# Kernel tuning notes

Hardware: AMD Instinct MI355X
Metric: run time of the kernel (lower is better)

Reference implementation:

```python
import jax, jax.numpy as jnp
import numpy as np
import math

SCORE_THRESH = 0.05
NMS_THRESH = 0.5
DETS_PER_IMG = 100
IMG_W = 512.0
IMG_H = 512.0
BBOX_XFORM_CLIP = math.log(1000.0 / 16.0)
WEIGHTS = (10.0, 10.0, 5.0, 5.0)
NEG_INF = jnp.float32(-1e30)


def decode(rel, boxes):
    TO_REMOVE = 1.0
    w = boxes[:, 2] - boxes[:, 0] + TO_REMOVE
    h = boxes[:, 3] - boxes[:, 1] + TO_REMOVE
    cx = boxes[:, 0] + 0.5 * w
    cy = boxes[:, 1] + 0.5 * h
    wx, wy, ww, wh = WEIGHTS
    dx = rel[:, 0::4] / wx
    dy = rel[:, 1::4] / wy
    dw = jnp.minimum(rel[:, 2::4] / ww, BBOX_XFORM_CLIP)
    dh = jnp.minimum(rel[:, 3::4] / wh, BBOX_XFORM_CLIP)
    pcx = dx * w[:, None] + cx[:, None]
    pcy = dy * h[:, None] + cy[:, None]
    pw = jnp.exp(dw) * w[:, None]
    ph = jnp.exp(dh) * h[:, None]
    x1 = pcx - 0.5 * pw
    y1 = pcy - 0.5 * ph
    x2 = pcx + 0.5 * pw - 1.0
    y2 = pcy + 0.5 * ph - 1.0
    return jnp.stack([x1, y1, x2, y2], axis=-1)


def pairwise_iou(b):
    # b: [N,4] xyxy -> [N,N] IoU (with +1 box-size convention, matching _box_nms)
    area = (b[:, 2] - b[:, 0] + 1.0) * (b[:, 3] - b[:, 1] + 1.0)
    xx1 = jnp.maximum(b[:, None, 0], b[None, :, 0])
    yy1 = jnp.maximum(b[:, None, 1], b[None, :, 1])
    xx2 = jnp.minimum(b[:, None, 2], b[None, :, 2])
    yy2 = jnp.minimum(b[:, None, 3], b[None, :, 3])
    inter = jnp.maximum(xx2 - xx1 + 1.0, 0.0) * jnp.maximum(yy2 - yy1 + 1.0, 0.0)
    return inter / (area[:, None] + area[None, :] - inter)


def _process_image(logits, regr, props):
    # logits: [N,2], regr: [N,8], props: [N,4]
    N = logits.shape[0]
    probs = jax.nn.softmax(logits, axis=-1)
    dec = decode(regr, props)            # [N, 2, 4]
    boxes = dec[:, 1, :]                  # fg (lesion) class boxes
    scores = probs[:, 1]                  # fg scores
    # clip_to_image(remove_empty=False)
    boxes = jnp.stack([
        jnp.clip(boxes[:, 0], 0.0, IMG_W - 1.0),
        jnp.clip(boxes[:, 1], 0.0, IMG_H - 1.0),
        jnp.clip(boxes[:, 2], 0.0, IMG_W - 1.0),
        jnp.clip(boxes[:, 3], 0.0, IMG_H - 1.0)], axis=-1)
    valid = scores > SCORE_THRESH
    # sort by score descending, invalid (below-threshold) boxes last
    order = jnp.argsort(-jnp.where(valid, scores, NEG_INF))
    boxes_s = boxes[order]
    scores_s = scores[order]
    valid_s = valid[order]
    iou = pairwise_iou(boxes_s)           # [N,N]
    idxs = jnp.arange(N)
    def body(i, keep):
        # box i (if still kept) suppresses all later overlapping boxes
        sup = keep[i] & (iou[i] > NMS_THRESH) & (idxs > i)
        return keep & ~sup
    keep = jax.lax.fori_loop(0, N, body, valid_s)
    # keep top detections_per_img by score among surviving boxes
    final = jnp.where(keep, scores_s, NEG_INF)
    top_scores, top_idx = jax.lax.top_k(final, DETS_PER_IMG)
    top_valid = keep[top_idx]
    top_boxes = jnp.where(top_valid[:, None], boxes_s[top_idx], 0.0)
    top_scores = jnp.where(top_valid, top_scores, 0.0)
    out = jnp.concatenate([top_boxes, top_scores[:, None]], axis=-1)  # [D, 5]
    labels = jnp.where(top_valid, 1, 0).astype(jnp.int32)
    return out, labels, top_valid


def setup_inputs() -> dict:
    key = jax.random.key(0)
    kl, kr, kp = jax.random.split(key, 3)
    B, N = 16, 4096
    class_logits = jax.random.normal(kl, (B, N, 2), dtype=jnp.float32)
    box_regression = jax.random.normal(kr, (B, N, 8), dtype=jnp.float32)
    raw = jax.random.uniform(kp, (B, N, 4), dtype=jnp.float32)
    x1 = raw[..., 0] * (IMG_W - 72.0)
    y1 = raw[..., 1] * (IMG_H - 72.0)
    bw = raw[..., 2] * 56.0 + 8.0
    bh = raw[..., 3] * 56.0 + 8.0
    proposals = jnp.stack([x1, y1, x1 + bw, y1 + bh], axis=-1)
    return {"class_logits": class_logits, "box_regression": box_regression, "proposals": proposals}


def reference(class_logits, box_regression, proposals):
    # returns (detections [B, D, 5] = xyxy+score, labels [B, D], valid [B, D])
    return jax.vmap(_process_image)(class_logits, box_regression, proposals)
```

## Files before the change

### kernel.cpp

```cpp
#include <hip/hip_runtime.h>
#include <math.h>

#define NTHREADS 512
#define MAXN 4096
#define PER 8
#define DETS 100
#define CHUNK 256
#define CAP 512
#define NWAVES (NTHREADS / 64)

static __device__ __forceinline__ unsigned long long shfl_bc64(unsigned long long x, int src) {
    int lo = __shfl((int)(unsigned)x, src, 64);
    int hi = __shfl((int)(unsigned)(x >> 32), src, 64);
    return ((unsigned long long)(unsigned)hi << 32) | (unsigned)lo;
}

static __device__ __forceinline__ float iou_f(float ax1, float ay1, float ax2, float ay2, float aar,
                                              float bx1, float by1, float bx2, float by2, float bar) {
#pragma clang fp contract(off)
    float xx1 = fmaxf(ax1, bx1), yy1 = fmaxf(ay1, by1);
    float xx2 = fminf(ax2, bx2), yy2 = fminf(ay2, by2);
    float iw = fmaxf((xx2 - xx1) + 1.0f, 0.0f);
    float ih = fmaxf((yy2 - yy1) + 1.0f, 0.0f);
    float inter = iw * ih;
    return inter / ((aar + bar) - inter);
}

__global__ __launch_bounds__(NTHREADS) void postproc_kernel(
    const float* __restrict__ logits,
    const float* __restrict__ regr,
    const float* __restrict__ props,
    float* __restrict__ out,
    int B, int N)
{
#pragma clang fp contract(off)
    const int b    = blockIdx.x;
    const int tid  = threadIdx.x;
    const int lane = tid & 63;
    const int wid  = tid >> 6;

    __shared__ __align__(16) unsigned long long keysel[CAP];
    __shared__ unsigned hist4k[4096];
    __shared__ unsigned s_super[64];
    __shared__ float bx1s[CAP], by1s[CAP], bx2s[CAP], by2s[CAP], bars[CAP], bscs[CAP];
    __shared__ float kb[5][DETS + 64];
    __shared__ unsigned tmask[64][2];
    __shared__ unsigned supk[64];
    __shared__ int s_kept, s_cnt, s_C;
    __shared__ unsigned long long s_prefix, s_T;
    __shared__ int s_target, s_done, s_findkey;

    const float* lg = logits + (size_t)b * N * 2;
    const float* rg = regr   + (size_t)b * N * 8;
    const float* pp = props  + (size_t)b * N * 4;

    unsigned long long v[PER];
#pragma unroll
    for (int s = 0; s < PER; ++s) {
        int a = s * NTHREADS + tid;
        unsigned long long key;
        if (a < N) {
            float2 l = ((const float2*)lg)[a];
            float zmax = fmaxf(l.x, l.y), zmin = fminf(l.x, l.y);
            float e   = (float)exp((double)(zmin - zmax));
            float den = e + 1.0f;
            float sscore = (l.y >= l.x) ? (1.0f / den) : (e / den);
            float f = (sscore > 0.05f) ? sscore : -1e30f;
            unsigned u = __float_as_uint(f);
            u = (u & 0x80000000u) ? ~u : (u | 0x80000000u);
            key = ((unsigned long long)(~u) << 32) | (unsigned)a;
        } else key = ~0ull;
        v[s] = key;
    }
    if (tid == 0) s_kept = 0;

    float* obox = out + (size_t)b * DETS * 5;
    float* olab = out + (size_t)B * DETS * 5 + (size_t)b * DETS;
    float* oval = out + (size_t)B * DETS * 5 + (size_t)B * DETS + (size_t)b * DETS;
    const float CLIPV = (float)4.135166556742356;

    int kept = 0;

    while (kept < DETS) {
        for (int i = tid; i < 4096; i += NTHREADS) hist4k[i] = 0u;
        if (tid == 0) { s_cnt = 0; s_C = 0; }
        __syncthreads();

#pragma unroll
        for (int s = 0; s < PER; ++s) {
            unsigned hb = (unsigned)(v[s] >> 50) - 0x1000u;
            if (hb > 4094u) hb = 4095u;
            atomicAdd(&hist4k[hb], 1u);
        }
        __syncthreads();

        {
            unsigned p = 0;
            int base8 = tid * 8;
#pragma unroll
            for (int u = 0; u < 8; ++u) p += hist4k[base8 + u];
#pragma unroll
            for (int off = 4; off; off >>= 1) p += __shfl_down(p, off, 8);
            if ((tid & 7) == 0) s_super[tid >> 3] = p;
        }
        __syncthreads();

        if (tid < 64) {
            int l = tid;
            int sp = (int)s_super[l];
            int incl = sp;
#pragma unroll
            for (int off = 1; off < 64; off <<= 1) {
                int y = __shfl_up(incl, off, 64);
                if (l >= off) incl += y;
            }
            int total = __shfl(incl, 63, 64);
            int inv   = (int)hist4k[4095];
            int W     = total - inv;
            if (W > 0) {
                int tgt2 = W < CHUNK ? W : CHUNK;
                int excl = incl - sp;
                bool hit = (excl < tgt2) && (tgt2 <= incl);
                unsigned long long bm = __ballot(hit);
                int E = __ffsll(bm) - 1;
                int prevCum = __shfl(excl, E, 64);
                int c2 = (int)hist4k[E * 64 + l];
                int incl2 = c2;
#pragma unroll
                for (int off = 1; off < 64; off <<= 1) {
                    int y = __shfl_up(incl2, off, 64);
                    if (l >= off) incl2 += y;
                }
                int cum2 = prevCum + incl2;
                int excl2 = cum2 - c2;
                bool hit2 = (excl2 < tgt2) && (tgt2 <= cum2);
                if (hit2) {
                    int bin = E * 64 + l;
                    unsigned k32end = ((0x1000u + (unsigned)bin + 1u) << 18) - 1u;
                    s_T = ((unsigned long long)k32end << 32) | 0xFFFFFFFFull;
                    s_C = cum2;
                    s_target = tgt2;
                }
            }
        }
        __syncthreads();
        int C = s_C;
        if (C == 0) break;

        if (C > CAP) {
            unsigned (*histw)[256] = (unsigned(*)[256])hist4k;
            if (tid == 0) { s_prefix = 0ull; s_done = 0; s_findkey = 0; }
            for (int round = 0; round < 10; ++round) {
                __syncthreads();
                if (s_done) break;
                int sh = 56 - 8 * round;
                if (s_findkey) {
                    unsigned long long want = s_prefix; int shh = sh + 8;
#pragma unroll
                    for (int s = 0; s < PER; ++s)
                        if ((v[s] >> shh) == want) { s_T = v[s]; s_done = 1; }
                    continue;
                }
                for (int i = tid; i < NWAVES * 256; i += NTHREADS) ((unsigned*)histw)[i] = 0u;
                __syncthreads();
                unsigned long long pfx = s_prefix;
#pragma unroll
                for (int s = 0; s < PER; ++s) {
                    unsigned long long k = v[s];
                    bool match = (round == 0) || ((k >> (sh + 8)) == pfx);
                    if (match) atomicAdd(&histw[wid][(unsigned)((k >> sh) & 0xFFull)], 1u);
                }
                __syncthreads();
                if (tid < 64) {
                    int l = tid;
                    unsigned c0 = 0, c1 = 0, c2 = 0, c3 = 0;
#pragma unroll
                    for (int w2 = 0; w2 < NWAVES; ++w2) {
                        c0 += histw[w2][4*l+0]; c1 += histw[w2][4*l+1];
                        c2 += histw[w2][4*l+2]; c3 += histw[w2][4*l+3];
                    }
                    unsigned q0 = c0, q1 = q0 + c1, q2 = q1 + c2, q3 = q2 + c3;
                    int lanesum = (int)q3, incl = lanesum;
#pragma unroll
                    for (int off = 1; off < 64; off <<= 1) {
                        int y = __shfl_up(incl, off, 64);
                        if (l >= off) incl += y;
                    }
                    unsigned excl = (unsigned)(incl - lanesum);
                    unsigned tg = (unsigned)s_target;
                    if ((excl < tg) && (tg <= (unsigned)incl)) {
                        unsigned within = tg - excl;
                        int u_; unsigned below, bc;
                        if      (within <= q0) { u_ = 0; below = excl;      bc = c0; }
                        else if (within <= q1) { u_ = 1; below = excl + q0; bc = c1; }
                        else if (within <= q2) { u_ = 2; below = excl + q1; bc = c2; }
                        else                   { u_ = 3; below = excl + q2; bc = c3; }
                        unsigned long long npfx = (pfx << 8) | (unsigned)(4*l + u_);
                        s_target = (int)(tg - below);
                        if (sh == 0) { s_T = npfx; s_done = 1; }
                        else { s_prefix = npfx; if (bc == 1u) s_findkey = 1; }
                    }
                }
            }
            __syncthreads();
        }
        unsigned long long T = s_T;

#pragma unroll
        for (int s = 0; s < PER; ++s) {
            unsigned long long k = v[s];
            bool m = (k <= T);
            unsigned long long mask = __ballot(m);
            int basep = 0;
            if (lane == 0 && mask) basep = atomicAdd(&s_cnt, (int)__popcll(mask));
            basep = __shfl(basep, 0, 64);
            if (m) {
                int off = (int)__popcll(mask & ((1ull << lane) - 1ull));
                keysel[basep + off] = k;
                v[s] = ~0ull;
            }
        }
        __syncthreads();
        int cnt = s_cnt;

        if (tid < cnt) {
            unsigned long long myk = keysel[tid];
            unsigned idx = (unsigned)(myk & 0xFFFFFFFFull);
            float2 l  = ((const float2*)lg)[idx];
            float4 p  = ((const float4*)pp)[idx];
            float4 rr = *(const float4*)(rg + (size_t)idx * 8 + 4);
            int r = 0;
            const ulonglong2* kp2 = (const ulonglong2*)keysel;
            int half = cnt >> 1;
            for (int j = 0; j < half; ++j) {
                ulonglong2 two = kp2[j];
                r += (two.x < myk) ? 1 : 0;
                r += (two.y < myk) ? 1 : 0;
            }
            if (cnt & 1) r += (keysel[cnt - 1] < myk) ? 1 : 0;
            float zmax = fmaxf(l.x, l.y), zmin = fminf(l.x, l.y);
            float e = (float)exp((double)(zmin - zmax));
            float den = e + 1.0f;
            float sv = (l.y >= l.x) ? (1.0f / den) : (e / den);
            float w  = (p.z - p.x) + 1.0f;
            float h  = (p.w - p.y) + 1.0f;
            float cx = p.x + 0.5f * w;
            float cy = p.y + 0.5f * h;
            float dx = rr.x / 10.0f;
            float dy = rr.y / 10.0f;
            float dw = fminf(rr.z / 5.0f, CLIPV);
            float dh = fminf(rr.w / 5.0f, CLIPV);
            float pcx = dx * w + cx;
            float pcy = dy * h + cy;
            float ew = (float)exp((double)dw);
            float eh = (float)exp((double)dh);
            float pw = ew * w;
            float ph = eh * h;
            float x1 = pcx - 0.5f * pw;
            float y1 = pcy - 0.5f * ph;
            float x2 = (pcx + 0.5f * pw) - 1.0f;
            float y2 = (pcy + 0.5f * ph) - 1.0f;
            x1 = fminf(fmaxf(x1, 0.0f), 511.0f);
            y1 = fminf(fmaxf(y1, 0.0f), 511.0f);
            x2 = fminf(fmaxf(x2, 0.0f), 511.0f);
            y2 = fminf(fmaxf(y2, 0.0f), 511.0f);
            bx1s[r] = x1; by1s[r] = y1; bx2s[r] = x2; by2s[r] = y2;
            bars[r] = ((x2 - x1) + 1.0f) * ((y2 - y1) + 1.0f);
            bscs[r] = sv;
        }
        __syncthreads();

        for (int i0 = 0; i0 < cnt && kept < DETS; i0 += 64) {
            if (tid < 64) supk[tid] = (i0 + tid < cnt) ? 0u : 1u;
            else if (tid < 192) { int q = tid - 64; tmask[q >> 1][q & 1] = 0u; }
            __syncthreads();

            {
                int cc = tid & 63, sl = tid >> 6;
                if (supk[cc] == 0u) {
                    int gi = i0 + cc;
                    float x1 = bx1s[gi], y1 = by1s[gi], x2 = bx2s[gi], y2 = by2s[gi], ar = bars[gi];
                    for (int s2 = sl; s2 < kept; s2 += 8) {
                        float iou = iou_f(kb[0][s2], kb[1][s2], kb[2][s2], kb[3][s2], kb[4][s2],
                                          x1, y1, x2, y2, ar);
                        if (iou > 0.5f) { supk[cc] = 1u; break; }
                    }
                }
            }
            {
                int i = tid >> 3, jb = (tid & 7) << 3;
                int gi = i0 + i;
                float x1 = bx1s[gi], y1 = by1s[gi], x2 = bx2s[gi], y2 = by2s[gi], ar = bars[gi];
                unsigned byte = 0;
#pragma unroll
                for (int u = 0; u < 8; ++u) {
                    int j = jb + u;
                    if (j > i) {
                        int gj = i0 + j;
                        float iou = iou_f(x1, y1, x2, y2, ar,
                                          bx1s[gj], by1s[gj], bx2s[gj], by2s[gj], bars[gj]);
                        if (iou > 0.5f) byte |= (1u << u);
                    }
                }
                if (byte) atomicOr(&tmask[i][jb >> 5], byte << (jb & 31));
            }
            __syncthreads();

            if (tid < 64) {
                int l = tid;
                unsigned long long row = ((unsigned long long)tmask[l][1] << 32) | tmask[l][0];
                int alive0 = supk[l] ? 0 : 1;
                unsigned long long aliveMask = __ballot(alive0);
                unsigned long long pend = __ballot(alive0 && row != 0ull);
                while (pend) {
                    int c = __ffsll(pend) - 1;
                    unsigned long long rc = shfl_bc64(row, c);
                    aliveMask &= ~rc;
                    pend &= ~(1ull << c);
                    pend &= aliveMask;
                }
                int alive = (int)((aliveMask >> l) & 1ull);
                int rank = kept + (int)__popcll(aliveMask & ((1ull << l) - 1ull));
                int gi = i0 + l;
                if (alive) {
                    if (rank < DETS) {
                        float* o = obox + rank * 5;
                        o[0] = bx1s[gi]; o[1] = by1s[gi]; o[2] = bx2s[gi]; o[3] = by2s[gi];
                        o[4] = bscs[gi];
                        olab[rank] = 1.0f;
                        oval[rank] = 1.0f;
                    }
                    kb[0][rank] = bx1s[gi]; kb[1][rank] = by1s[gi];
                    kb[2][rank] = bx2s[gi]; kb[3][rank] = by2s[gi];
                    kb[4][rank] = bars[gi];
                }
                if (l == 0) s_kept = kept + (int)__popcll(aliveMask);
            }
            __syncthreads();
            kept = s_kept;
        }
    }

    int start = kept < DETS ? kept : DETS;
    for (int c2 = start + tid; c2 < DETS; c2 += NTHREADS) {
        float* o = obox + c2 * 5;
        o[0] = 0.0f; o[1] = 0.0f; o[2] = 0.0f; o[3] = 0.0f; o[4] = 0.0f;
        olab[c2] = 0.0f;
        oval[c2] = 0.0f;
    }
}

extern "C" void kernel_launch(void* const* d_in, const int* in_sizes, int n_in,
                              void* d_out, int out_size, void* d_ws, size_t ws_size,
                              hipStream_t stream) {
    (void)d_ws; (void)ws_size; (void)n_in;
    const float* logits = (const float*)d_in[0];
    const float* regr   = (const float*)d_in[1];
    const float* props  = (const float*)d_in[2];
    float* out = (float*)d_out;

    int B = out_size / 700;
    if (B < 1) B = 1;
    int N = in_sizes[0] / (2 * B);

    postproc_kernel<<<B, NTHREADS, 0, stream>>>(logits, regr, props, out, B, N);
}
```

Before: 21.26 us.

## Process whole 256-candidate chunk with single IoU matrix and bitmask NMS pass

Replaces the per-64-candidate NMS sub-loop with one pass over the entire candidate chunk (up to 256). All threads build a 256x256 upper-triangular suppression bitmask and check against already-kept boxes in the same barrier phase, and a single wave then resolves survivors with early exit once 100 detections are reached. The threshold selection now picks the largest bin prefix that fits within the chunk, falling back to the radix refine only when the first bin alone overflows. This cuts barrier rounds and serial chunk iterations, at the cost of more IoU work per chunk and 64-bit shared atomics.

```diff
diff --git a/kernel.cpp b/kernel.cpp
--- a/kernel.cpp
+++ b/kernel.cpp
@@ -5,15 +5,8 @@
 #define MAXN 4096
 #define PER 8
 #define DETS 100
-#define CHUNK 256
-#define CAP 512
+#define CMAX 256
 #define NWAVES (NTHREADS / 64)
-
-static __device__ __forceinline__ unsigned long long shfl_bc64(unsigned long long x, int src) {
-    int lo = __shfl((int)(unsigned)x, src, 64);
-    int hi = __shfl((int)(unsigned)(x >> 32), src, 64);
-    return ((unsigned long long)(unsigned)hi << 32) | (unsigned)lo;
-}
 
 static __device__ __forceinline__ float iou_f(float ax1, float ay1, float ax2, float ay2, float aar,
                                               float bx1, float by1, float bx2, float by2, float bar) {
@@ -39,14 +32,15 @@
     const int lane = tid & 63;
     const int wid  = tid >> 6;
 
-    __shared__ __align__(16) unsigned long long keysel[CAP];
+    __shared__ __align__(16) unsigned long long keysel[CMAX];
     __shared__ unsigned hist4k[4096];
     __shared__ unsigned s_super[64];
-    __shared__ float bx1s[CAP], by1s[CAP], bx2s[CAP], by2s[CAP], bars[CAP], bscs[CAP];
-    __shared__ float kb[5][DETS + 64];
-    __shared__ unsigned tmask[64][2];
-    __shared__ unsigned supk[64];
-    __shared__ int s_kept, s_cnt, s_C;
+    __shared__ unsigned long long rowmask[CMAX][4];
+    __shared__ unsigned rowNZ[CMAX];
+    __shared__ unsigned supk[CMAX];
+    __shared__ float bx1s[CMAX], by1s[CMAX], bx2s[CMAX], by2s[CMAX], bars[CMAX], bscs[CMAX];
+    __shared__ float kb[5][DETS + 4];
+    __shared__ int s_kept, s_cnt, s_C, s_fb;
     __shared__ unsigned long long s_prefix, s_T;
     __shared__ int s_target, s_done, s_findkey;
 
@@ -83,7 +77,7 @@
 
     while (kept < DETS) {
         for (int i = tid; i < 4096; i += NTHREADS) hist4k[i] = 0u;
-        if (tid == 0) { s_cnt = 0; s_C = 0; }
+        if (tid == 0) { s_cnt = 0; s_C = 0; s_fb = 0; }
         __syncthreads();
 
 #pragma unroll
@@ -107,47 +101,55 @@
 
         if (tid < 64) {
             int l = tid;
-            int sp = (int)s_super[l];
+            int inv = (int)hist4k[4095];
+            int sp = (int)s_super[l] - ((l == 63) ? inv : 0);
             int incl = sp;
 #pragma unroll
             for (int off = 1; off < 64; off <<= 1) {
                 int y = __shfl_up(incl, off, 64);
                 if (l >= off) incl += y;
             }
-            int total = __shfl(incl, 63, 64);
-            int inv   = (int)hist4k[4095];
-            int W     = total - inv;
+            int W = __shfl(incl, 63, 64);
             if (W > 0) {
-                int tgt2 = W < CHUNK ? W : CHUNK;
+                int tgt2 = W < CMAX ? W : CMAX;
                 int excl = incl - sp;
-                bool hit = (excl < tgt2) && (tgt2 <= incl);
+                bool hit = (excl <= tgt2) && (incl > tgt2);
                 unsigned long long bm = __ballot(hit);
-                int E = __ffsll(bm) - 1;
-                int prevCum = __shfl(excl, E, 64);
-                int c2 = (int)hist4k[E * 64 + l];
-                int incl2 = c2;
-#pragma unroll
-                for (int off = 1; off < 64; off <<= 1) {
-                    int y = __shfl_up(incl2, off, 64);
-                    if (l >= off) incl2 += y;
-                }
-                int cum2 = prevCum + incl2;
-                int excl2 = cum2 - c2;
-                bool hit2 = (excl2 < tgt2) && (tgt2 <= cum2);
-                if (hit2) {
-                    int bin = E * 64 + l;
-                    unsigned k32end = ((0x1000u + (unsigned)bin + 1u) << 18) - 1u;
-                    s_T = ((unsigned long long)k32end << 32) | 0xFFFFFFFFull;
-                    s_C = cum2;
-                    s_target = tgt2;
-                }
-            }
-        }
-        __syncthreads();
-        int C = s_C;
-        if (C == 0) break;
-
-        if (C > CAP) {
+                if (bm == 0ull) {
+                    if (l == 0) {
+                        s_C = W;
+                        s_T = ((unsigned long long)0x7FFBFFFFu << 32) | 0xFFFFFFFFull;
+                    }
+                } else {
+                    int E = (int)(__ffsll(bm) - 1);
+                    int prevCum = __shfl(excl, E, 64);
+                    int c2 = (E == 63 && l == 63) ? 0 : (int)hist4k[E * 64 + l];
+                    int incl2 = c2;
+#pragma unroll
+                    for (int off = 1; off < 64; off <<= 1) {
+                        int y = __shfl_up(incl2, off, 64);
+                        if (l >= off) incl2 += y;
+                    }
+                    int cum = prevCum + incl2;
+                    unsigned long long okm = __ballot(cum <= tgt2);
+                    int q = (int)__popcll(okm);
+                    int Cq = (q > 0) ? __shfl(cum, q - 1, 64) : prevCum;
+                    if (l == 0) {
+                        if (Cq == 0) { s_fb = 1; s_target = tgt2; }
+                        else {
+                            int bin = E * 64 + q - 1;
+                            unsigned k32end = ((0x1000u + (unsigned)bin + 1u) << 18) - 1u;
+                            s_T = ((unsigned long long)k32end << 32) | 0xFFFFFFFFull;
+                            s_C = Cq;
+                        }
+                    }
+                }
+            }
+        }
+        __syncthreads();
+        if (!s_fb && s_C == 0) break;
+
+        if (s_fb) {
             unsigned (*histw)[256] = (unsigned(*)[256])hist4k;
             if (tid == 0) { s_prefix = 0ull; s_done = 0; s_findkey = 0; }
             for (int round = 0; round < 10; ++round) {
@@ -221,7 +223,7 @@
             }
         }
         __syncthreads();
-        int cnt = s_cnt;
+        const int cnt = s_cnt;
 
         if (tid < cnt) {
             unsigned long long myk = keysel[tid];
@@ -267,78 +269,119 @@
             bx1s[r] = x1; by1s[r] = y1; bx2s[r] = x2; by2s[r] = y2;
             bars[r] = ((x2 - x1) + 1.0f) * ((y2 - y1) + 1.0f);
             bscs[r] = sv;
-        }
-        __syncthreads();
-
-        for (int i0 = 0; i0 < cnt && kept < DETS; i0 += 64) {
-            if (tid < 64) supk[tid] = (i0 + tid < cnt) ? 0u : 1u;
-            else if (tid < 192) { int q = tid - 64; tmask[q >> 1][q & 1] = 0u; }
-            __syncthreads();
-
-            {
-                int cc = tid & 63, sl = tid >> 6;
-                if (supk[cc] == 0u) {
-                    int gi = i0 + cc;
-                    float x1 = bx1s[gi], y1 = by1s[gi], x2 = bx2s[gi], y2 = by2s[gi], ar = bars[gi];
-                    for (int s2 = sl; s2 < kept; s2 += 8) {
+        } else if (tid >= CMAX) {
+            int z = tid - CMAX;
+            rowmask[z][0] = 0ull; rowmask[z][1] = 0ull;
+            rowmask[z][2] = 0ull; rowmask[z][3] = 0ull;
+            rowNZ[z] = 0u; supk[z] = 0u;
+        }
+        __syncthreads();
+
+        {
+            int q = tid >> 2, sub = tid & 3;
+            int i = (sub < 2) ? q : (CMAX - 1 - q);
+            if (i < cnt) {
+                float x1 = bx1s[i], y1 = by1s[i], x2 = bx2s[i], y2 = by2s[i], ar = bars[i];
+                unsigned long long acc0 = 0, acc1 = 0, acc2 = 0, acc3 = 0;
+                for (int j = i + 1 + (sub & 1); j < cnt; j += 2) {
+                    float iou = iou_f(x1, y1, x2, y2, ar,
+                                      bx1s[j], by1s[j], bx2s[j], by2s[j], bars[j]);
+                    if (iou > 0.5f) {
+                        unsigned long long bit = 1ull << (j & 63);
+                        int wq = j >> 6;
+                        if (wq == 0) acc0 |= bit; else if (wq == 1) acc1 |= bit;
+                        else if (wq == 2) acc2 |= bit; else acc3 |= bit;
+                    }
+                }
+                unsigned long long any = acc0 | acc1 | acc2 | acc3;
+                if (any) {
+                    if (acc0) atomicOr(&rowmask[i][0], acc0);
+                    if (acc1) atomicOr(&rowmask[i][1], acc1);
+                    if (acc2) atomicOr(&rowmask[i][2], acc2);
+                    if (acc3) atomicOr(&rowmask[i][3], acc3);
+                    rowNZ[i] = 1u;
+                }
+            }
+            if (kept > 0) {
+                int c = tid & (CMAX - 1), sl = tid >> 8;
+                if (c < cnt) {
+                    float x1 = bx1s[c], y1 = by1s[c], x2 = bx2s[c], y2 = by2s[c], ar = bars[c];
+                    for (int s2 = sl; s2 < kept; s2 += 2) {
                         float iou = iou_f(kb[0][s2], kb[1][s2], kb[2][s2], kb[3][s2], kb[4][s2],
                                           x1, y1, x2, y2, ar);
-                        if (iou > 0.5f) { supk[cc] = 1u; break; }
-                    }
-                }
-            }
-            {
-                int i = tid >> 3, jb = (tid & 7) << 3;
-                int gi = i0 + i;
-                float x1 = bx1s[gi], y1 = by1s[gi], x2 = bx2s[gi], y2 = by2s[gi], ar = bars[gi];
-                unsigned byte = 0;
-#pragma unroll
-                for (int u = 0; u < 8; ++u) {
-                    int j = jb + u;
-                    if (j > i) {
-                        int gj = i0 + j;
-                        float iou = iou_f(x1, y1, x2, y2, ar,
-                                          bx1s[gj], by1s[gj], bx2s[gj], by2s[gj], bars[gj]);
-                        if (iou > 0.5f) byte |= (1u << u);
-                    }
-                }
-                if (byte) atomicOr(&tmask[i][jb >> 5], byte << (jb & 31));
-            }
-            __syncthreads();
-
-            if (tid < 64) {
-                int l = tid;
-                unsigned long long row = ((unsigned long long)tmask[l][1] << 32) | tmask[l][0];
-                int alive0 = supk[l] ? 0 : 1;
-                unsigned long long aliveMask = __ballot(alive0);
-                unsigned long long pend = __ballot(alive0 && row != 0ull);
-                while (pend) {
-                    int c = __ffsll(pend) - 1;
-                    unsigned long long rc = shfl_bc64(row, c);
-                    aliveMask &= ~rc;
-                    pend &= ~(1ull << c);
-                    pend &= aliveMask;
-                }
-                int alive = (int)((aliveMask >> l) & 1ull);
-                int rank = kept + (int)__popcll(aliveMask & ((1ull << l) - 1ull));
-                int gi = i0 + l;
-                if (alive) {
+                        if (iou > 0.5f) { supk[c] = 1u; break; }
+                    }
+                }
+            }
+        }
+        __syncthreads();
+
+        if (tid < 64) {
+            int l = tid;
+            unsigned long long alive[4], pend[4];
+#pragma unroll
+            for (int w = 0; w < 4; ++w) {
+                int c = w * 64 + l;
+                bool a  = (c < cnt) && (supk[c] == 0u);
+                alive[w] = __ballot(a);
+                pend[w]  = __ballot(a && (rowNZ[c] != 0u));
+            }
+            int fin = CMAX;
+            for (;;) {
+                int w_ = pend[0] ? 0 : pend[1] ? 1 : pend[2] ? 2 : pend[3] ? 3 : -1;
+                if (w_ < 0) break;
+                int cb = (int)(__ffsll(pend[w_]) - 1);
+                int c  = w_ * 64 + cb;
+                int below = 0;
+#pragma unroll
+                for (int w = 0; w < 4; ++w)
+                    if (w < w_) below += (int)__popcll(alive[w]);
+                below += (int)__popcll(alive[w_] & ((1ull << cb) - 1ull));
+                if (kept + below >= DETS) { fin = c; break; }
+                unsigned long long r0 = rowmask[c][0], r1 = rowmask[c][1];
+                unsigned long long r2 = rowmask[c][2], r3 = rowmask[c][3];
+                alive[0] &= ~r0; alive[1] &= ~r1; alive[2] &= ~r2; alive[3] &= ~r3;
+                pend[w_] &= ~(1ull << cb);
+                pend[0] &= alive[0]; pend[1] &= alive[1];
+                pend[2] &= alive[2]; pend[3] &= alive[3];
+            }
+            unsigned long long finA[4];
+#pragma unroll
+            for (int w = 0; w < 4; ++w) {
+                int lo = w * 64;
+                unsigned long long m;
+                if (fin >= lo + 64) m = ~0ull;
+                else if (fin <= lo) m = 0ull;
+                else m = (1ull << (fin - lo)) - 1ull;
+                finA[w] = alive[w] & m;
+            }
+            int pc0 = (int)__popcll(finA[0]);
+            int pc1 = (int)__popcll(finA[1]);
+            int pc2 = (int)__popcll(finA[2]);
+            int pc3 = (int)__popcll(finA[3]);
+            int tot = pc0 + pc1 + pc2 + pc3;
+            int pref[4] = {0, pc0, pc0 + pc1, pc0 + pc1 + pc2};
+#pragma unroll
+            for (int w = 0; w < 4; ++w) {
+                int c = w * 64 + l;
+                if ((finA[w] >> l) & 1ull) {
+                    int rank = kept + pref[w] + (int)__popcll(finA[w] & ((1ull << l) - 1ull));
                     if (rank < DETS) {
                         float* o = obox + rank * 5;
-                        o[0] = bx1s[gi]; o[1] = by1s[gi]; o[2] = bx2s[gi]; o[3] = by2s[gi];
-                        o[4] = bscs[gi];
+                        float X1 = bx1s[c], Y1 = by1s[c], X2 = bx2s[c], Y2 = by2s[c];
+                        o[0] = X1; o[1] = Y1; o[2] = X2; o[3] = Y2; o[4] = bscs[c];
                         olab[rank] = 1.0f;
                         oval[rank] = 1.0f;
-                    }
-                    kb[0][rank] = bx1s[gi]; kb[1][rank] = by1s[gi];
-                    kb[2][rank] = bx2s[gi]; kb[3][rank] = by2s[gi];
-                    kb[4][rank] = bars[gi];
-                }
-                if (l == 0) s_kept = kept + (int)__popcll(aliveMask);
-            }
-            __syncthreads();
-            kept = s_kept;
-        }
+                        kb[0][rank] = X1; kb[1][rank] = Y1;
+                        kb[2][rank] = X2; kb[3][rank] = Y2;
+                        kb[4][rank] = bars[c];
+                    }
+                }
+            }
+            if (l == 0) s_kept = kept + tot;
+        }
+        __syncthreads();
+        kept = s_kept;
     }
 
     int start = kept < DETS ? kept : DETS;
```

New measurement: 33.86 us. +59.3%, slower.

## Shrink radix-select histogram to 256 bins and vectorize logit loads

Applied to the files above, without the earlier changes.

Replaces the 4096-bin histogram and its two-level prefix scan with a 256-bin histogram (larger bins clamp into an overflow bucket) scanned by a single wave, with each lane holding four bins. When the selected bin holds more than CAP candidates it falls back to the existing multi-round radix refinement. Logits are loaded as float4, two proposals per load. This cuts histogram clearing, scan work and barriers per round, but coarser bins may send more iterations down the fallback path.

```diff
diff --git a/kernel.cpp b/kernel.cpp
--- a/kernel.cpp
+++ b/kernel.cpp
@@ -24,6 +24,18 @@
     float ih = fmaxf((yy2 - yy1) + 1.0f, 0.0f);
     float inter = iw * ih;
     return inter / ((aar + bar) - inter);
+}
+
+static __device__ __forceinline__ unsigned long long make_key(float lx, float ly, int a) {
+#pragma clang fp contract(off)
+    float zmax = fmaxf(lx, ly), zmin = fminf(lx, ly);
+    float e   = (float)exp((double)(zmin - zmax));
+    float den = e + 1.0f;
+    float sscore = (ly >= lx) ? (1.0f / den) : (e / den);
+    float f = (sscore > 0.05f) ? sscore : -1e30f;
+    unsigned u = __float_as_uint(f);
+    u = (u & 0x80000000u) ? ~u : (u | 0x80000000u);
+    return ((unsigned long long)(~u) << 32) | (unsigned)a;
 }
 
 __global__ __launch_bounds__(NTHREADS) void postproc_kernel(
@@ -40,13 +52,12 @@
     const int wid  = tid >> 6;
 
     __shared__ __align__(16) unsigned long long keysel[CAP];
-    __shared__ unsigned hist4k[4096];
-    __shared__ unsigned s_super[64];
+    __shared__ unsigned hist[2048];
     __shared__ float bx1s[CAP], by1s[CAP], bx2s[CAP], by2s[CAP], bars[CAP], bscs[CAP];
     __shared__ float kb[5][DETS + 64];
     __shared__ unsigned tmask[64][2];
     __shared__ unsigned supk[64];
-    __shared__ int s_kept, s_cnt, s_C;
+    __shared__ int s_kept, s_cnt, s_C, s_fb;
     __shared__ unsigned long long s_prefix, s_T;
     __shared__ int s_target, s_done, s_findkey;
 
@@ -55,22 +66,19 @@
     const float* pp = props  + (size_t)b * N * 4;
 
     unsigned long long v[PER];
-#pragma unroll
-    for (int s = 0; s < PER; ++s) {
-        int a = s * NTHREADS + tid;
-        unsigned long long key;
-        if (a < N) {
-            float2 l = ((const float2*)lg)[a];
-            float zmax = fmaxf(l.x, l.y), zmin = fminf(l.x, l.y);
-            float e   = (float)exp((double)(zmin - zmax));
-            float den = e + 1.0f;
-            float sscore = (l.y >= l.x) ? (1.0f / den) : (e / den);
-            float f = (sscore > 0.05f) ? sscore : -1e30f;
-            unsigned u = __float_as_uint(f);
-            u = (u & 0x80000000u) ? ~u : (u | 0x80000000u);
-            key = ((unsigned long long)(~u) << 32) | (unsigned)a;
-        } else key = ~0ull;
-        v[s] = key;
+    const float4* lg4 = (const float4*)lg;
+#pragma unroll
+    for (int s = 0; s < PER / 2; ++s) {
+        int L = s * NTHREADS + tid;
+        int a0 = 2 * L, a1 = 2 * L + 1;
+        if (a1 < N) {
+            float4 q = lg4[L];
+            v[2*s]   = make_key(q.x, q.y, a0);
+            v[2*s+1] = make_key(q.z, q.w, a1);
+        } else {
+            v[2*s]   = (a0 < N) ? make_key(lg[2*a0], lg[2*a0+1], a0) : ~0ull;
+            v[2*s+1] = ~0ull;
+        }
     }
     if (tid == 0) s_kept = 0;
 
@@ -82,73 +90,55 @@
     int kept = 0;
 
     while (kept < DETS) {
-        for (int i = tid; i < 4096; i += NTHREADS) hist4k[i] = 0u;
-        if (tid == 0) { s_cnt = 0; s_C = 0; }
+        if (tid < 256) hist[tid] = 0u;
+        if (tid == 0) { s_cnt = 0; s_C = 0; s_fb = 0; }
         __syncthreads();
 
 #pragma unroll
         for (int s = 0; s < PER; ++s) {
             unsigned hb = (unsigned)(v[s] >> 50) - 0x1000u;
-            if (hb > 4094u) hb = 4095u;
-            atomicAdd(&hist4k[hb], 1u);
-        }
-        __syncthreads();
-
-        {
-            unsigned p = 0;
-            int base8 = tid * 8;
-#pragma unroll
-            for (int u = 0; u < 8; ++u) p += hist4k[base8 + u];
-#pragma unroll
-            for (int off = 4; off; off >>= 1) p += __shfl_down(p, off, 8);
-            if ((tid & 7) == 0) s_super[tid >> 3] = p;
+            if (hb > 2047u) hb = 2047u;
+            atomicAdd(&hist[hb], 1u);
         }
         __syncthreads();
 
         if (tid < 64) {
             int l = tid;
-            int sp = (int)s_super[l];
-            int incl = sp;
+            unsigned c0 = hist[4*l+0], c1 = hist[4*l+1], c2 = hist[4*l+2], c3 = hist[4*l+3];
+            unsigned q0 = c0, q1 = q0 + c1, q2 = q1 + c2, q3 = q2 + c3;
+            int lanesum = (int)q3, incl = lanesum;
 #pragma unroll
             for (int off = 1; off < 64; off <<= 1) {
                 int y = __shfl_up(incl, off, 64);
                 if (l >= off) incl += y;
             }
-            int total = __shfl(incl, 63, 64);
-            int inv   = (int)hist4k[4095];
-            int W     = total - inv;
+            int excl = incl - lanesum;
+            int W = __shfl(incl, 63, 64);
             if (W > 0) {
                 int tgt2 = W < CHUNK ? W : CHUNK;
-                int excl = incl - sp;
-                bool hit = (excl < tgt2) && (tgt2 <= incl);
-                unsigned long long bm = __ballot(hit);
-                int E = __ffsll(bm) - 1;
-                int prevCum = __shfl(excl, E, 64);
-                int c2 = (int)hist4k[E * 64 + l];
-                int incl2 = c2;
-#pragma unroll
-                for (int off = 1; off < 64; off <<= 1) {
-                    int y = __shfl_up(incl2, off, 64);
-                    if (l >= off) incl2 += y;
-                }
-                int cum2 = prevCum + incl2;
-                int excl2 = cum2 - c2;
-                bool hit2 = (excl2 < tgt2) && (tgt2 <= cum2);
-                if (hit2) {
-                    int bin = E * 64 + l;
-                    unsigned k32end = ((0x1000u + (unsigned)bin + 1u) << 18) - 1u;
-                    s_T = ((unsigned long long)k32end << 32) | 0xFFFFFFFFull;
-                    s_C = cum2;
-                    s_target = tgt2;
-                }
-            }
-        }
-        __syncthreads();
-        int C = s_C;
-        if (C == 0) break;
-
-        if (C > CAP) {
-            unsigned (*histw)[256] = (unsigned(*)[256])hist4k;
+                if (excl < tgt2 && tgt2 <= incl) {
+                    int within = tgt2 - excl;
+                    int u_; unsigned cq;
+                    if      (within <= (int)q0) { u_ = 0; cq = q0; }
+                    else if (within <= (int)q1) { u_ = 1; cq = q1; }
+                    else if (within <= (int)q2) { u_ = 2; cq = q2; }
+                    else                        { u_ = 3; cq = q3; }
+                    int C = excl + (int)cq;
+                    if (C > CAP) { s_fb = 1; s_target = tgt2; }
+                    else {
+                        int bin = 4 * l + u_;
+                        unsigned k32end = ((0x1000u + (unsigned)bin + 1u) << 18) - 1u;
+                        s_T = ((unsigned long long)k32end << 32) | 0xFFFFFFFFull;
+                        s_C = C;
+                    }
+                }
+            }
+        }
+        __syncthreads();
+        if (!s_fb && s_C == 0) break;
+
+        if (s_fb) {
+            unsigned (*histw)[256] = (unsigned(*)[256])hist;
             if (tid == 0) { s_prefix = 0ull; s_done = 0; s_findkey = 0; }
             for (int round = 0; round < 10; ++round) {
                 __syncthreads();
```

New measurement: 20.61 us. -3.0%, faster.
